# Kernel tuning notes

Measured on AMD Instinct MI355X. Metric: run time of the kernel, lower is better.

The kernel has to match this reference:

```python
import jax, jax.numpy as jnp
import numpy as np

LN_EPS = 1e-5

def setup_inputs() -> dict:
    key = jax.random.key(0)
    B, T, D, H, NB = 32, 384, 512, 16, 5  # NB = 5 MHSA blocks actually used
    ks = jax.random.split(key, 10)
    s = 1.0 / np.sqrt(D)
    def w(k, shape):
        return jax.random.normal(k, shape, jnp.float32) * s
    return {
        "x": jax.random.normal(ks[0], (B, T, D), jnp.float32),
        # stacked params for the 5 used MHSA blocks, order:
        # [tmp_attn, layer1_1, layer1_2, layer1_3, layer2_1]
        "qw": w(ks[1], (NB, D, D)), "qb": w(ks[2], (NB, D)),
        "kw": w(ks[3], (NB, D, D)), "kb": w(ks[4], (NB, D)),
        "vw": w(ks[5], (NB, D, D)), "vb": w(ks[6], (NB, D)),
        "temp": jnp.ones((NB, H, 1, 1), jnp.float32),
        "ln_g": jnp.ones((D,), jnp.float32),
        "ln_b": jnp.zeros((D,), jnp.float32),
        "fus_w": w(ks[7], (D, D)), "fus_b": w(ks[8], (D,)),
        "num_heads": H,
    }


def _mhsa(x, wq, bq, wk, bk, wv, bv, temp, H):
    # Faithful to torch: .view(B, H, D//H, T) is a flat reshape of (B,T,D).
    B, T, D = x.shape
    d = D // H
    q = (x @ wq.T + bq).reshape(B, H, d, T)
    k = (x @ wk.T + bk).reshape(B, H, d, T)
    v = (x @ wv.T + bv).reshape(B, H, d, T)
    # k^T @ v -> (B,H,T,T), scaled by per-head temperature, softmax over last dim
    attn = jax.nn.softmax(jnp.einsum("bhdt,bhds->bhts", k, v) * temp, axis=-1)
    out = jnp.einsum("bhdt,bhts->bhds", q, attn)  # (B,H,d,T)
    return out.reshape(B, T, D)


def _layernorm(x, g, b):
    mu = jnp.mean(x, axis=-1, keepdims=True)
    var = jnp.mean(jnp.square(x - mu), axis=-1, keepdims=True)
    return (x - mu) * jax.lax.rsqrt(var + LN_EPS) * g + b


def reference(x, qw, qb, kw, kb, vw, vb, temp, ln_g, ln_b, fus_w, fus_b, num_heads):
    H = num_heads
    blk = lambda i, z: _mhsa(z, qw[i], qb[i], kw[i], kb[i], vw[i], vb[i], temp[i], H)
    x_ = blk(0, x)
    c1, c2, c3 = jnp.split(x, 3, axis=1)
    tmp_layer1 = jnp.concatenate([blk(1, c1), blk(2, c2), blk(3, c3)], axis=1) + x_
    tmp_layer2 = blk(4, _layernorm(tmp_layer1, ln_g, ln_b)) + x_
    alpha = jnp.stack([tmp_layer1, tmp_layer2], axis=0)  # (2,B,T,D)
    alpha = alpha @ fus_w.T + fus_b
    alpha = jax.nn.softmax(alpha, axis=0)
    return tmp_layer1 * alpha[0] + tmp_layer2 * alpha[1]
```

## Files before the change

### kernel.cpp

```cpp
#include <hip/hip_runtime.h>

typedef __attribute__((ext_vector_type(8))) _Float16 half8;
typedef __attribute__((ext_vector_type(4))) _Float16 half4v;
typedef __attribute__((ext_vector_type(2))) _Float16 half2v;
typedef __attribute__((ext_vector_type(4))) float float4v;

__device__ __forceinline__ float4v mfma16x16x32_f16(half8 a, half8 b, float4v c) {
#if defined(__HIP_DEVICE_COMPILE__)
#if __has_builtin(__builtin_amdgcn_mfma_f32_16x16x32_f16)
  return __builtin_amdgcn_mfma_f32_16x16x32_f16(a, b, c, 0, 0, 0);
#elif __has_builtin(__builtin_amdgcn_mfma_f32_16x16x32f16)
  return __builtin_amdgcn_mfma_f32_16x16x32f16(a, b, c, 0, 0, 0);
#else
#error "no 16x16x32 f16 mfma"
#endif
#else
  (void)a; (void)b;
  return c;
#endif
}

__device__ __forceinline__ float4v mfma16x16x16_f16(half4v a, half4v b, float4v c) {
#if defined(__HIP_DEVICE_COMPILE__)
#if __has_builtin(__builtin_amdgcn_mfma_f32_16x16x16f16)
  return __builtin_amdgcn_mfma_f32_16x16x16f16(a, b, c, 0, 0, 0);
#elif __has_builtin(__builtin_amdgcn_mfma_f32_16x16x16_f16)
  return __builtin_amdgcn_mfma_f32_16x16x16_f16(a, b, c, 0, 0, 0);
#else
#error "no 16x16x16 f16 mfma"
#endif
#else
  (void)a; (void)b;
  return c;
#endif
}

__device__ __forceinline__ void gl_lds16(const unsigned short* g, unsigned short* l) {
#if defined(__HIP_DEVICE_COMPILE__)
#if __has_builtin(__builtin_amdgcn_global_load_lds)
  __builtin_amdgcn_global_load_lds(
      (const __attribute__((address_space(1))) unsigned int*)g,
      (__attribute__((address_space(3))) unsigned int*)l, 16, 0, 0);
#else
  *(uint4*)l = *(const uint4*)g;
#endif
#else
  (void)g; (void)l;
#endif
}

__device__ __forceinline__ float fexp2(float x) {
#if defined(__HIP_DEVICE_COMPILE__)
#if __has_builtin(__builtin_amdgcn_exp2f)
  return __builtin_amdgcn_exp2f(x);
#else
  return __expf(x * 0.6931471805599453f);
#endif
#else
  return x;
#endif
}

__device__ __forceinline__ float frcp(float x) {
#if defined(__HIP_DEVICE_COMPILE__)
#if __has_builtin(__builtin_amdgcn_rcpf)
  return __builtin_amdgcn_rcpf(x);
#else
  return 1.0f / x;
#endif
#else
  return 1.0f / x;
#endif
}

__device__ __forceinline__ half2v pk_f16(float a, float b) {
#if defined(__HIP_DEVICE_COMPILE__)
#if __has_builtin(__builtin_amdgcn_cvt_pkrtz)
  return __builtin_bit_cast(half2v, __builtin_amdgcn_cvt_pkrtz(a, b));
#else
  half2v r;
  r[0] = (_Float16)a;
  r[1] = (_Float16)b;
  return r;
#endif
#else
  half2v r;
  r[0] = (_Float16)a;
  r[1] = (_Float16)b;
  return r;
#endif
}

template <int P>
__device__ __forceinline__ void setprio() {
#if defined(__HIP_DEVICE_COMPILE__)
#if __has_builtin(__builtin_amdgcn_s_setprio)
  __builtin_amdgcn_s_setprio(P);
#endif
#endif
}

__device__ __forceinline__ unsigned short f2h(float f) {
  union { _Float16 h; unsigned short u; } v;
  v.h = (_Float16)f;
  return v.u;
}

__device__ __forceinline__ float row_sum16(float x) {
#if defined(__HIP_DEVICE_COMPILE__)
#if __has_builtin(__builtin_amdgcn_update_dpp)
  int v;
  v = __builtin_bit_cast(int, x);
  x += __builtin_bit_cast(float, __builtin_amdgcn_update_dpp(0, v, 0x128, 0xF, 0xF, true));
  v = __builtin_bit_cast(int, x);
  x += __builtin_bit_cast(float, __builtin_amdgcn_update_dpp(0, v, 0x124, 0xF, 0xF, true));
  v = __builtin_bit_cast(int, x);
  x += __builtin_bit_cast(float, __builtin_amdgcn_update_dpp(0, v, 0x122, 0xF, 0xF, true));
  v = __builtin_bit_cast(int, x);
  x += __builtin_bit_cast(float, __builtin_amdgcn_update_dpp(0, v, 0x121, 0xF, 0xF, true));
  return x;
#else
  x += __shfl_xor(x, 1);
  x += __shfl_xor(x, 2);
  x += __shfl_xor(x, 4);
  x += __shfl_xor(x, 8);
  return x;
#endif
#else
  return x;
#endif
}

__global__ __launch_bounds__(256) void cvt_multi(
    const float* __restrict__ s0, unsigned short* __restrict__ d0, int n0,
    const float* __restrict__ s1, unsigned short* __restrict__ d1,
    const float* __restrict__ s2, unsigned short* __restrict__ d2,
    const float* __restrict__ s3, unsigned short* __restrict__ d3, int n13,
    const float* __restrict__ s4, unsigned short* __restrict__ d4, int n4c) {
  const int y = blockIdx.y;
  const float* s;
  unsigned short* d;
  int n;
  if (y == 0) { s = s0; d = d0; n = n0; }
  else if (y == 1) { s = s1; d = d1; n = n13; }
  else if (y == 2) { s = s2; d = d2; n = n13; }
  else if (y == 3) { s = s3; d = d3; n = n13; }
  else { s = s4; d = d4; n = n4c; }
  const int i = blockIdx.x * 256 + threadIdx.x;
  if (i >= n) return;
  float4 v = ((const float4*)s)[i];
  uint2 o;
  o.x = (unsigned)f2h(v.x) | ((unsigned)f2h(v.y) << 16);
  o.y = (unsigned)f2h(v.z) | ((unsigned)f2h(v.w) << 16);
  ((uint2*)d)[i] = o;
}

#define GEMM_CORE(WGPTR)                                                               \
  for (int k0 = 0; k0 < 512; k0 += 64) {                                               \
    _Pragma("unroll") for (int rnd = 0; rnd < 2; ++rnd) {                              \
      const int slot = rnd * 512 + tid;                                                \
      const int r = slot >> 3;                                                         \
      const int c = (slot & 7) ^ (r & 7);                                              \
      gl_lds16(Xbase + xrow0 + (size_t)r * 512 + (size_t)(k0 + c * 8), &Xs[slot * 8]); \
    }                                                                                  \
    _Pragma("unroll") for (int rnd = 0; rnd < 2; ++rnd) {                              \
      const int s2 = rnd * 512 + tid;                                                  \
      const int r = s2 >> 3;                                                           \
      const int c = (s2 & 7) ^ (r & 7);                                                \
      gl_lds16((WGPTR) + (size_t)r * 512 + k0 + c * 8, &Wt[s2 * 8]);                   \
    }                                                                                  \
    __syncthreads();                                                                   \
    _Pragma("unroll") for (int kk = 0; kk < 2; ++kk) {                                 \
      half8 af[2], bf[4];                                                              \
      const int ch = ((kk * 4 + grp) ^ (col & 7)) * 8;                                 \
      _Pragma("unroll") for (int i = 0; i < 2; ++i)                                    \
          af[i] = *(const half8*)&Xs[(wm + i * 16 + col) * 64 + ch];                   \
      _Pragma("unroll") for (int j = 0; j < 4; ++j)                                    \
          bf[j] = *(const half8*)&Wt[(wn + j * 16 + col) * 64 + ch];                   \
      _Pragma("unroll") for (int i = 0; i < 2; ++i)                                    \
          _Pragma("unroll") for (int j = 0; j < 4; ++j)                                \
              acc[i][j] = mfma16x16x32_f16(af[i], bf[j], acc[i][j]);                   \
    }                                                                                  \
    __syncthreads();                                                                   \
  }

__global__ __launch_bounds__(512) void gemm_qkv6(
    const unsigned short* __restrict__ X,
    const unsigned short* __restrict__ Wq, const unsigned short* __restrict__ Wk,
    const unsigned short* __restrict__ Wv,
    const float* __restrict__ bq, const float* __restrict__ bk, const float* __restrict__ bv,
    unsigned short* __restrict__ CqA, unsigned short* __restrict__ CkA,
    unsigned short* __restrict__ CvA, unsigned short* __restrict__ CqB,
    unsigned short* __restrict__ CkB, unsigned short* __restrict__ CvB,
    int widx_fixed) {
  const int mt = blockIdx.x, nt = blockIdx.y, z = blockIdx.z;
  const int zz = z % 3, mode = z / 3;
  const unsigned short* W = (zz == 0) ? Wq : ((zz == 1) ? Wk : Wv);
  const float* bias = (zz == 0) ? bq : ((zz == 1) ? bk : bv);
  unsigned short* C = mode ? ((zz == 0) ? CqB : ((zz == 1) ? CkB : CvB))
                           : ((zz == 0) ? CqA : ((zz == 1) ? CkA : CvA));
  const int cpart = mt % 3, batch = mt / 3;
  const int widx = mode ? (1 + cpart) : widx_fixed;
  W += (size_t)widx * 512 * 512;
  bias += widx * 512;

  const size_t grow0 = (size_t)batch * 384 + cpart * 128;
  const size_t xrow0 = grow0 * 512;
  const unsigned short* Xbase = X;

  __shared__ __align__(16) unsigned short Xs[1024 * 8];
  __shared__ __align__(16) unsigned short Wt[1024 * 8];
  const int tid = threadIdx.x, lane = tid & 63, w = tid >> 6;
  const int col = lane & 15, grp = lane >> 4;
  const int wm = (w >> 1) * 32, wn = (w & 1) * 64;

  const float4v zero4 = {0.f, 0.f, 0.f, 0.f};
  float4v acc[2][4];
#pragma unroll
  for (int i = 0; i < 2; ++i)
#pragma unroll
    for (int j = 0; j < 4; ++j) acc[i][j] = zero4;

  GEMM_CORE(W + (size_t)nt * 128 * 512)

#pragma unroll
  for (int j = 0; j < 4; ++j) {
    const int n = nt * 128 + wn + j * 16 + col;
    const float bj = bias[n];
#pragma unroll
    for (int i = 0; i < 2; ++i)
#pragma unroll
      for (int r = 0; r < 4; ++r) {
        const int m = wm + i * 16 + grp * 4 + r;
        C[(grow0 + m) * 512 + n] = f2h(acc[i][j][r] + bj);
      }
  }
}

__global__ __launch_bounds__(512) void gemm_fusion(
    const unsigned short* __restrict__ X, const unsigned short* __restrict__ Wf,
    const float* __restrict__ dif, const float* __restrict__ tl2, float* __restrict__ outp) {
  const int mt = blockIdx.x, nt = blockIdx.y;
  const size_t grow0 = (size_t)mt * 128;
  const size_t xrow0 = grow0 * 512;
  const unsigned short* Xbase = X;

  __shared__ __align__(16) unsigned short Xs[1024 * 8];
  __shared__ __align__(16) unsigned short Wt[1024 * 8];
  const int tid = threadIdx.x, lane = tid & 63, w = tid >> 6;
  const int col = lane & 15, grp = lane >> 4;
  const int wm = (w >> 1) * 32, wn = (w & 1) * 64;

  const float4v zero4 = {0.f, 0.f, 0.f, 0.f};
  float4v acc[2][4];
#pragma unroll
  for (int i = 0; i < 2; ++i)
#pragma unroll
    for (int j = 0; j < 4; ++j) acc[i][j] = zero4;

  GEMM_CORE(Wf + (size_t)nt * 128 * 512)

#pragma unroll
  for (int j = 0; j < 4; ++j) {
    const int n = nt * 128 + wn + j * 16 + col;
#pragma unroll
    for (int i = 0; i < 2; ++i)
#pragma unroll
      for (int r = 0; r < 4; ++r) {
        const int m = wm + i * 16 + grp * 4 + r;
        const size_t off = (grow0 + m) * 512 + n;
        const float d = dif[off], t2 = tl2[off];
        const float sg = 1.0f / (1.0f + __expf(-acc[i][j][r]));
        outp[off] = t2 + d * sg;
      }
  }
}

template <int T, bool PRIO, bool VFIRST>
__device__ __forceinline__ void attn_body(
    const unsigned short* __restrict__ Qb, const unsigned short* __restrict__ Kb,
    const unsigned short* __restrict__ Vb, const float* __restrict__ temp_base,
    const float* add_src,
    float* outp, int chunk_elems, int cb, int h, int b,
    const float* tl1_src,
    unsigned short* diff16, float* diff32,
    unsigned short* KVt, float* Zs) {
  constexpr int NT = T / 16;
  constexpr int NSW = NT / 8;
  constexpr int SLAB = T * 32;
  const int base = b * (384 * 512) + cb * chunk_elems + h * SLAB;
  const float tl2e = temp_base[cb * 16 + h] * 1.4426950408889634f;

  const int tid = threadIdx.x, lane = tid & 63, w = tid >> 6;
  const int col = lane & 15, grp = lane >> 4;

  if (tid < NT * 16) Zs[tid] = 0.f;

  half8 vfr[NSW];
  auto load_v = [&]() {
    const unsigned short* Vg = Vb + base;
#pragma unroll
    for (int si = 0; si < NSW; ++si) {
      const int s = (w + si * 8) * 16 + col;
      union { unsigned short u[8]; half8 v; } t8;
#pragma unroll
      for (int i = 0; i < 8; ++i) t8.u[i] = Vg[(size_t)(grp * 8 + i) * T + s];
      vfr[si] = t8.v;
    }
  };
  auto stage_k = [&]() {
    const unsigned short* src = Kb + base;
    constexpr int ITER = (T * 4) / 512;
#pragma unroll
    for (int p = 0; p < ITER; ++p) {
      const int f = p * 512 + tid;
      const int t = f >> 2, blk = (f & 3) * 8;
      unsigned short tmp[8];
#pragma unroll
      for (int i = 0; i < 8; ++i) tmp[i] = src[(size_t)(blk + i) * T + t];
      *(uint4*)&KVt[t * 40 + blk] = *(const uint4*)tmp;
    }
  };
  if constexpr (VFIRST) {
    load_v();
    stage_k();
  } else {
    stage_k();
    load_v();
  }
  __syncthreads();

  const float4v zero4 = {0.f, 0.f, 0.f, 0.f};

#pragma unroll 2
  for (int tt = 0; tt < NT; ++tt) {
    half8 kf = *(const half8*)&KVt[(tt * 16 + col) * 40 + grp * 8];
    float z0 = 0.f, z1 = 0.f, z2 = 0.f, z3 = 0.f;
    if constexpr (PRIO) setprio<1>();
#pragma unroll
    for (int si = 0; si < NSW; ++si) {
      float4v sv = mfma16x16x32_f16(kf, vfr[si], zero4);
      z0 += fexp2(sv[0] * tl2e);
      z1 += fexp2(sv[1] * tl2e);
      z2 += fexp2(sv[2] * tl2e);
      z3 += fexp2(sv[3] * tl2e);
    }
    if constexpr (PRIO) setprio<0>();
    z0 = row_sum16(z0);
    z1 = row_sum16(z1);
    z2 = row_sum16(z2);
    z3 = row_sum16(z3);
    if (col == 0) {
      float* zp = &Zs[tt * 16 + grp * 4];
      atomicAdd(zp + 0, z0);
      atomicAdd(zp + 1, z1);
      atomicAdd(zp + 2, z2);
      atomicAdd(zp + 3, z3);
    }
  }
  __syncthreads();

  const unsigned short* Qsl = Qb + base;
  float4v oacc[NSW][2];
#pragma unroll
  for (int si = 0; si < NSW; ++si) {
    oacc[si][0] = zero4;
    oacc[si][1] = zero4;
  }
#pragma unroll 2
  for (int tt = 0; tt < NT; ++tt) {
    const int toff = tt * 16 + grp * 4;
    half4v qa0 = *(const half4v*)(Qsl + col * T + toff);
    half4v qa1 = *(const half4v*)(Qsl + (16 + col) * T + toff);
    float4v zsv = *(const float4v*)&Zs[tt * 16 + grp * 4];
    const float zi0 = frcp(zsv[0]), zi1 = frcp(zsv[1]), zi2 = frcp(zsv[2]),
                zi3 = frcp(zsv[3]);
    half8 kf = *(const half8*)&KVt[(tt * 16 + col) * 40 + grp * 8];
    if constexpr (PRIO) setprio<1>();
#pragma unroll
    for (int si = 0; si < NSW; ++si) {
      float4v sv = mfma16x16x32_f16(kf, vfr[si], zero4);
      half2v lo = pk_f16(fexp2(sv[0] * tl2e) * zi0, fexp2(sv[1] * tl2e) * zi1);
      half2v hi = pk_f16(fexp2(sv[2] * tl2e) * zi2, fexp2(sv[3] * tl2e) * zi3);
      half4v pb = __builtin_shufflevector(lo, hi, 0, 1, 2, 3);
      oacc[si][0] = mfma16x16x16_f16(qa0, pb, oacc[si][0]);
      oacc[si][1] = mfma16x16x16_f16(qa1, pb, oacc[si][1]);
    }
    if constexpr (PRIO) setprio<0>();
  }

#pragma unroll
  for (int si = 0; si < NSW; ++si) {
    const int s = (w + si * 8) * 16 + col;
#pragma unroll
    for (int m0 = 0; m0 < 2; ++m0) {
#pragma unroll
      for (int r = 0; r < 4; ++r) {
        const int dd = m0 * 16 + grp * 4 + r;
        const int off = base + dd * T + s;
        const float o = oacc[si][m0][r];
        float v = o;
        if (add_src) v += add_src[off];
        if (tl1_src) {
          const float d = tl1_src[off] - o;
          diff16[off] = f2h(d);
          diff32[off] = d;
        }
        outp[off] = v;
      }
    }
  }
}

__global__ __launch_bounds__(512) void attn_merged(
    const unsigned short* __restrict__ Q0, const unsigned short* __restrict__ K0,
    const unsigned short* __restrict__ V0, const unsigned short* __restrict__ Qc,
    const unsigned short* __restrict__ Kc, const unsigned short* __restrict__ Vc,
    const float* __restrict__ temp, float* xres, float* tl1) {
  __shared__ __align__(16) unsigned short Ks[384 * 40];
  __shared__ __align__(16) float Zs[24 * 16];
  const int id = blockIdx.x + 16 * (blockIdx.y + 32 * blockIdx.z);
  if (id < 512) {
    const int h = id & 15, b = id >> 4;
    attn_body<384, true, true>(Q0, K0, V0, temp, nullptr, xres, 0, 0, h, b,
                               nullptr, nullptr, nullptr, Ks, Zs);
  } else {
    const int idl = id - 512;
    const int cb = idl >> 9;
    const int rest = idl & 511;
    const int h = rest & 15, b = rest >> 4;
    attn_body<128, true, true>(Qc, Kc, Vc, temp + 16, nullptr, tl1, 128 * 512,
                               cb, h, b, nullptr, nullptr, nullptr, Ks, Zs);
  }
}

__global__ __launch_bounds__(512) void attn_tail(
    const unsigned short* __restrict__ Q, const unsigned short* __restrict__ K,
    const unsigned short* __restrict__ V, const float* __restrict__ temp4,
    const float* add_src, float* tl12, unsigned short* __restrict__ diff16,
    float* diff32) {
  __shared__ __align__(16) unsigned short Ks[384 * 40];
  __shared__ __align__(16) float Zs[24 * 16];
  attn_body<384, false, false>(Q, K, V, temp4, add_src, tl12, 0, 0, blockIdx.x,
                               blockIdx.y, tl12, diff16, diff32, Ks, Zs);
}

__global__ __launch_bounds__(256) void ln_kernel(const float* __restrict__ a,
                                                 const float* __restrict__ c,
                                                 const float* __restrict__ g,
                                                 const float* __restrict__ bb,
                                                 unsigned short* __restrict__ y) {
  const int row = blockIdx.x * 4 + (threadIdx.x >> 6);
  const int lane = threadIdx.x & 63;
  const float* ar = a + (size_t)row * 512;
  const float* cr = c + (size_t)row * 512;
  float4 a0 = *(const float4*)&ar[lane * 8];
  float4 a1 = *(const float4*)&ar[lane * 8 + 4];
  float4 c0 = *(const float4*)&cr[lane * 8];
  float4 c1 = *(const float4*)&cr[lane * 8 + 4];
  float4 v0, v1;
  v0.x = a0.x + c0.x; v0.y = a0.y + c0.y; v0.z = a0.z + c0.z; v0.w = a0.w + c0.w;
  v1.x = a1.x + c1.x; v1.y = a1.y + c1.y; v1.z = a1.z + c1.z; v1.w = a1.w + c1.w;
  float s = v0.x + v0.y + v0.z + v0.w + v1.x + v1.y + v1.z + v1.w;
  float q = v0.x * v0.x + v0.y * v0.y + v0.z * v0.z + v0.w * v0.w +
            v1.x * v1.x + v1.y * v1.y + v1.z * v1.z + v1.w * v1.w;
#pragma unroll
  for (int m = 1; m < 64; m <<= 1) {
    s += __shfl_xor(s, m);
    q += __shfl_xor(q, m);
  }
  const float mean = s * (1.0f / 512.0f);
  const float var = q * (1.0f / 512.0f) - mean * mean;
  const float rs = rsqrtf(var + 1e-5f);
  float4 g0 = *(const float4*)&g[lane * 8];
  float4 g1 = *(const float4*)&g[lane * 8 + 4];
  float4 b0 = *(const float4*)&bb[lane * 8];
  float4 b1 = *(const float4*)&bb[lane * 8 + 4];
  uint4 o;
  o.x = (unsigned)f2h((v0.x - mean) * rs * g0.x + b0.x) |
        ((unsigned)f2h((v0.y - mean) * rs * g0.y + b0.y) << 16);
  o.y = (unsigned)f2h((v0.z - mean) * rs * g0.z + b0.z) |
        ((unsigned)f2h((v0.w - mean) * rs * g0.w + b0.w) << 16);
  o.z = (unsigned)f2h((v1.x - mean) * rs * g1.x + b1.x) |
        ((unsigned)f2h((v1.y - mean) * rs * g1.y + b1.y) << 16);
  o.w = (unsigned)f2h((v1.z - mean) * rs * g1.z + b1.z) |
        ((unsigned)f2h((v1.w - mean) * rs * g1.w + b1.w) << 16);
  *(uint4*)&y[(size_t)row * 512 + lane * 8] = o;
}

extern "C" void kernel_launch(void* const* d_in, const int* in_sizes, int n_in,
                              void* d_out, int out_size, void* d_ws, size_t ws_size,
                              hipStream_t stream) {
  const float* x = (const float*)d_in[0];
  const float* qw = (const float*)d_in[1];
  const float* qb = (const float*)d_in[2];
  const float* kw = (const float*)d_in[3];
  const float* kb = (const float*)d_in[4];
  const float* vw = (const float*)d_in[5];
  const float* vb = (const float*)d_in[6];
  const float* temp = (const float*)d_in[7];
  const float* ln_g = (const float*)d_in[8];
  const float* ln_b = (const float*)d_in[9];
  const float* fus_w = (const float*)d_in[10];
  float* out = (float*)d_out;

  const size_t NE = (size_t)32 * 384 * 512;
  const size_t WE = (size_t)5 * 512 * 512;

  char* p = (char*)d_ws;
  auto alloc = [&](size_t bytes) {
    char* r = p;
    p += (bytes + 255) & ~(size_t)255;
    return r;
  };
  unsigned short* xb = (unsigned short*)alloc(NE * 2);
  unsigned short* wqb = (unsigned short*)alloc(WE * 2);
  unsigned short* wkb = (unsigned short*)alloc(WE * 2);
  unsigned short* wvb = (unsigned short*)alloc(WE * 2);
  unsigned short* fwb = (unsigned short*)alloc((size_t)512 * 512 * 2);
  unsigned short* Qb = (unsigned short*)alloc(NE * 2);
  unsigned short* Kb = (unsigned short*)alloc(NE * 2);
  unsigned short* Vb = (unsigned short*)alloc(NE * 2);
  float* xres = (float*)alloc(NE * 4);
  float* tl1 = (float*)alloc(NE * 4);
  unsigned short* yb = (unsigned short*)alloc(NE * 2);

  unsigned short* Qc = yb;
  unsigned short* Kc = (unsigned short*)out;
  unsigned short* Vc = Kc + NE;

  cvt_multi<<<dim3((int)(NE / 4 / 256), 5), 256, 0, stream>>>(
      x, xb, (int)(NE / 4), qw, wqb, kw, wkb, vw, wvb, (int)(WE / 4), fus_w, fwb,
      512 * 512 / 4);

  gemm_qkv6<<<dim3(96, 4, 6), 512, 0, stream>>>(xb, wqb, wkb, wvb, qb, kb, vb,
                                                Qb, Kb, Vb, Qc, Kc, Vc, 0);
  attn_merged<<<dim3(16, 32, 4), 512, 0, stream>>>(Qb, Kb, Vb, Qc, Kc, Vc, temp,
                                                   xres, tl1);
  ln_kernel<<<12288 / 4, 256, 0, stream>>>(tl1, xres, ln_g, ln_b, yb);
  gemm_qkv6<<<dim3(96, 4, 3), 512, 0, stream>>>(yb, wqb, wkb, wvb, qb, kb, vb,
                                                Qb, Kb, Vb, Qb, Kb, Vb, 4);
  attn_tail<<<dim3(16, 32, 1), 512, 0, stream>>>(Qb, Kb, Vb, temp + 64, xres, tl1,
                                                 yb, xres);
  gemm_fusion<<<dim3(96, 4), 512, 0, stream>>>(yb, fwb, xres, tl1, out);

  (void)in_sizes; (void)n_in; (void)out_size; (void)ws_size;
}
```

Baseline: 334.8 us.

## Fuse softmax denominator and PV passes in merged attention to avoid recomputing scores

```diff
diff --git a/kernel.cpp b/kernel.cpp
--- a/kernel.cpp
+++ b/kernel.cpp
@@ -276,7 +276,7 @@
   }
 }
 
-template <int T, bool PRIO, bool VFIRST>
+template <int T, bool PRIO, bool VFIRST, bool GROUPED>
 __device__ __forceinline__ void attn_body(
     const unsigned short* __restrict__ Qb, const unsigned short* __restrict__ Kb,
     const unsigned short* __restrict__ Vb, const float* __restrict__ temp_base,
@@ -331,35 +331,6 @@
   __syncthreads();
 
   const float4v zero4 = {0.f, 0.f, 0.f, 0.f};
-
-#pragma unroll 2
-  for (int tt = 0; tt < NT; ++tt) {
-    half8 kf = *(const half8*)&KVt[(tt * 16 + col) * 40 + grp * 8];
-    float z0 = 0.f, z1 = 0.f, z2 = 0.f, z3 = 0.f;
-    if constexpr (PRIO) setprio<1>();
-#pragma unroll
-    for (int si = 0; si < NSW; ++si) {
-      float4v sv = mfma16x16x32_f16(kf, vfr[si], zero4);
-      z0 += fexp2(sv[0] * tl2e);
-      z1 += fexp2(sv[1] * tl2e);
-      z2 += fexp2(sv[2] * tl2e);
-      z3 += fexp2(sv[3] * tl2e);
-    }
-    if constexpr (PRIO) setprio<0>();
-    z0 = row_sum16(z0);
-    z1 = row_sum16(z1);
-    z2 = row_sum16(z2);
-    z3 = row_sum16(z3);
-    if (col == 0) {
-      float* zp = &Zs[tt * 16 + grp * 4];
-      atomicAdd(zp + 0, z0);
-      atomicAdd(zp + 1, z1);
-      atomicAdd(zp + 2, z2);
-      atomicAdd(zp + 3, z3);
-    }
-  }
-  __syncthreads();
-
   const unsigned short* Qsl = Qb + base;
   float4v oacc[NSW][2];
 #pragma unroll
@@ -367,26 +338,112 @@
     oacc[si][0] = zero4;
     oacc[si][1] = zero4;
   }
+
+  if constexpr (GROUPED) {
+    for (int g = 0; g < NT / 2; ++g) {
+      float pe[2][NSW][4];
+#pragma unroll
+      for (int u = 0; u < 2; ++u) {
+        const int tt = g * 2 + u;
+        half8 kf = *(const half8*)&KVt[(tt * 16 + col) * 40 + grp * 8];
+        float z0 = 0.f, z1 = 0.f, z2 = 0.f, z3 = 0.f;
+        if constexpr (PRIO) setprio<1>();
+#pragma unroll
+        for (int si = 0; si < NSW; ++si) {
+          float4v sv = mfma16x16x32_f16(kf, vfr[si], zero4);
+          pe[u][si][0] = fexp2(sv[0] * tl2e);
+          pe[u][si][1] = fexp2(sv[1] * tl2e);
+          pe[u][si][2] = fexp2(sv[2] * tl2e);
+          pe[u][si][3] = fexp2(sv[3] * tl2e);
+          z0 += pe[u][si][0];
+          z1 += pe[u][si][1];
+          z2 += pe[u][si][2];
+          z3 += pe[u][si][3];
+        }
+        if constexpr (PRIO) setprio<0>();
+        z0 = row_sum16(z0);
+        z1 = row_sum16(z1);
+        z2 = row_sum16(z2);
+        z3 = row_sum16(z3);
+        if (col == 0) {
+          float* zp = &Zs[tt * 16 + grp * 4];
+          atomicAdd(zp + 0, z0);
+          atomicAdd(zp + 1, z1);
+          atomicAdd(zp + 2, z2);
+          atomicAdd(zp + 3, z3);
+        }
+      }
+      __syncthreads();
+#pragma unroll
+      for (int u = 0; u < 2; ++u) {
+        const int tt = g * 2 + u;
+        const int toff = tt * 16 + grp * 4;
+        half4v qa0 = *(const half4v*)(Qsl + col * T + toff);
+        half4v qa1 = *(const half4v*)(Qsl + (16 + col) * T + toff);
+        float4v zsv = *(const float4v*)&Zs[tt * 16 + grp * 4];
+        const float zi0 = frcp(zsv[0]), zi1 = frcp(zsv[1]), zi2 = frcp(zsv[2]),
+                    zi3 = frcp(zsv[3]);
+        if constexpr (PRIO) setprio<1>();
+#pragma unroll
+        for (int si = 0; si < NSW; ++si) {
+          half2v lo = pk_f16(pe[u][si][0] * zi0, pe[u][si][1] * zi1);
+          half2v hi = pk_f16(pe[u][si][2] * zi2, pe[u][si][3] * zi3);
+          half4v pb = __builtin_shufflevector(lo, hi, 0, 1, 2, 3);
+          oacc[si][0] = mfma16x16x16_f16(qa0, pb, oacc[si][0]);
+          oacc[si][1] = mfma16x16x16_f16(qa1, pb, oacc[si][1]);
+        }
+        if constexpr (PRIO) setprio<0>();
+      }
+    }
+  } else {
 #pragma unroll 2
-  for (int tt = 0; tt < NT; ++tt) {
-    const int toff = tt * 16 + grp * 4;
-    half4v qa0 = *(const half4v*)(Qsl + col * T + toff);
-    half4v qa1 = *(const half4v*)(Qsl + (16 + col) * T + toff);
-    float4v zsv = *(const float4v*)&Zs[tt * 16 + grp * 4];
-    const float zi0 = frcp(zsv[0]), zi1 = frcp(zsv[1]), zi2 = frcp(zsv[2]),
-                zi3 = frcp(zsv[3]);
-    half8 kf = *(const half8*)&KVt[(tt * 16 + col) * 40 + grp * 8];
-    if constexpr (PRIO) setprio<1>();
-#pragma unroll
-    for (int si = 0; si < NSW; ++si) {
-      float4v sv = mfma16x16x32_f16(kf, vfr[si], zero4);
-      half2v lo = pk_f16(fexp2(sv[0] * tl2e) * zi0, fexp2(sv[1] * tl2e) * zi1);
-      half2v hi = pk_f16(fexp2(sv[2] * tl2e) * zi2, fexp2(sv[3] * tl2e) * zi3);
-      half4v pb = __builtin_shufflevector(lo, hi, 0, 1, 2, 3);
-      oacc[si][0] = mfma16x16x16_f16(qa0, pb, oacc[si][0]);
-      oacc[si][1] = mfma16x16x16_f16(qa1, pb, oacc[si][1]);
+    for (int tt = 0; tt < NT; ++tt) {
+      half8 kf = *(const half8*)&KVt[(tt * 16 + col) * 40 + grp * 8];
+      float z0 = 0.f, z1 = 0.f, z2 = 0.f, z3 = 0.f;
+      if constexpr (PRIO) setprio<1>();
+#pragma unroll
+      for (int si = 0; si < NSW; ++si) {
+        float4v sv = mfma16x16x32_f16(kf, vfr[si], zero4);
+        z0 += fexp2(sv[0] * tl2e);
+        z1 += fexp2(sv[1] * tl2e);
+        z2 += fexp2(sv[2] * tl2e);
+        z3 += fexp2(sv[3] * tl2e);
+      }
+      if constexpr (PRIO) setprio<0>();
+      z0 = row_sum16(z0);
+      z1 = row_sum16(z1);
+      z2 = row_sum16(z2);
+      z3 = row_sum16(z3);
+      if (col == 0) {
+        float* zp = &Zs[tt * 16 + grp * 4];
+        atomicAdd(zp + 0, z0);
+        atomicAdd(zp + 1, z1);
+        atomicAdd(zp + 2, z2);
+        atomicAdd(zp + 3, z3);
+      }
     }
-    if constexpr (PRIO) setprio<0>();
+    __syncthreads();
+#pragma unroll 2
+    for (int tt = 0; tt < NT; ++tt) {
+      const int toff = tt * 16 + grp * 4;
+      half4v qa0 = *(const half4v*)(Qsl + col * T + toff);
+      half4v qa1 = *(const half4v*)(Qsl + (16 + col) * T + toff);
+      float4v zsv = *(const float4v*)&Zs[tt * 16 + grp * 4];
+      const float zi0 = frcp(zsv[0]), zi1 = frcp(zsv[1]), zi2 = frcp(zsv[2]),
+                  zi3 = frcp(zsv[3]);
+      half8 kf = *(const half8*)&KVt[(tt * 16 + col) * 40 + grp * 8];
+      if constexpr (PRIO) setprio<1>();
+#pragma unroll
+      for (int si = 0; si < NSW; ++si) {
+        float4v sv = mfma16x16x32_f16(kf, vfr[si], zero4);
+        half2v lo = pk_f16(fexp2(sv[0] * tl2e) * zi0, fexp2(sv[1] * tl2e) * zi1);
+        half2v hi = pk_f16(fexp2(sv[2] * tl2e) * zi2, fexp2(sv[3] * tl2e) * zi3);
+        half4v pb = __builtin_shufflevector(lo, hi, 0, 1, 2, 3);
+        oacc[si][0] = mfma16x16x16_f16(qa0, pb, oacc[si][0]);
+        oacc[si][1] = mfma16x16x16_f16(qa1, pb, oacc[si][1]);
+      }
+      if constexpr (PRIO) setprio<0>();
+    }
   }
 
 #pragma unroll
@@ -422,15 +479,15 @@
   const int id = blockIdx.x + 16 * (blockIdx.y + 32 * blockIdx.z);
   if (id < 512) {
     const int h = id & 15, b = id >> 4;
-    attn_body<384, true, true>(Q0, K0, V0, temp, nullptr, xres, 0, 0, h, b,
-                               nullptr, nullptr, nullptr, Ks, Zs);
+    attn_body<384, true, true, true>(Q0, K0, V0, temp, nullptr, xres, 0, 0, h, b,
+                                     nullptr, nullptr, nullptr, Ks, Zs);
   } else {
     const int idl = id - 512;
     const int cb = idl >> 9;
     const int rest = idl & 511;
     const int h = rest & 15, b = rest >> 4;
-    attn_body<128, true, true>(Qc, Kc, Vc, temp + 16, nullptr, tl1, 128 * 512,
-                               cb, h, b, nullptr, nullptr, nullptr, Ks, Zs);
+    attn_body<128, true, true, true>(Qc, Kc, Vc, temp + 16, nullptr, tl1, 128 * 512,
+                                     cb, h, b, nullptr, nullptr, nullptr, Ks, Zs);
   }
 }
 
@@ -441,8 +498,9 @@
     float* diff32) {
   __shared__ __align__(16) unsigned short Ks[384 * 40];
   __shared__ __align__(16) float Zs[24 * 16];
-  attn_body<384, false, false>(Q, K, V, temp4, add_src, tl12, 0, 0, blockIdx.x,
-                               blockIdx.y, tl12, diff16, diff32, Ks, Zs);
+  attn_body<384, false, false, false>(Q, K, V, temp4, add_src, tl12, 0, 0,
+                                      blockIdx.x, blockIdx.y, tl12, diff16, diff32,
+                                      Ks, Zs);
 }
 
 __global__ __launch_bounds__(256) void ln_kernel(const float* __restrict__ a,
```

Measured after the change: 337.6 us. About the same (+0.8%).
